# Kernel optimization log

Measured on AMD Instinct MI355X. Metric: run time of the kernel, lower is better.

The kernel has to match this reference:

```python
import jax, jax.numpy as jnp
import numpy as np

DIST = 3.0
COEFF = 10.0
NEG_SLOPE = 0.3  # keras LeakyReLU default


def _probe_points(dist=DIST):
    # fixed 26 probe offsets on a sphere of radius `dist` (from build())
    angles = np.array(
        [[j * 0.125 - 0.125, i * 0.125 + (j - 1) * 0.0625] for j in range(3) for i in range(8)]
        + [[-0.25, 0.0], [0.25, 0.0]],
        dtype=np.float32,
    ) * (2.0 * np.pi)
    a, b = angles[:, 0], angles[:, 1]
    pts = np.stack([np.sin(a), np.cos(a) * np.cos(b), np.cos(a) * np.sin(b)], axis=-1) * dist
    return jnp.asarray(pts, dtype=jnp.float32)  # (26, 3)


def setup_inputs() -> dict:
    key = jax.random.key(0)
    k1, k2, k3 = jax.random.split(key, 3)
    B, n, f = 2, 1024, 3
    m, out_feats, num_convs = 26, 6, 5
    points = jax.random.normal(k1, (B, n, 3 + f), dtype=jnp.float32)
    # per-conv Dense(m*f -> out_feats) weights/bias, stacked over num_convs
    W = jax.random.normal(k2, (num_convs, m * f, out_feats), dtype=jnp.float32) * 0.1
    b = jax.random.normal(k3, (num_convs, out_feats), dtype=jnp.float32) * 0.1
    return {"points": points, "W": W, "b": b}


def reference(points, W, b):
    B, n, df = points.shape
    d = 3
    f = df - d
    probes = _probe_points()              # (m, d)
    m = probes.shape[0]
    coords = points[..., :d]              # (B, n, d) -> centers too (l = n)
    feats = points[..., d:]               # (B, n, f)
    centers = coords
    # probes per center: (B, l, m, d)
    probes_per_center = centers[:, :, None, :] + probes[None, None, :, :]
    # delta: (B, l, m, n, d)
    delta = coords[:, None, None, :, :] - probes_per_center[:, :, :, None, :]
    sq = jnp.sum(delta * delta, axis=-1)  # (B, l, m, n)
    wgt = COEFF / (sq + COEFF)            # inverse-distance weights
    # weighted feature sum: (B, l, m, f), averaged over n
    wf = jnp.einsum('blmn,bnf->blmf', wgt, feats) / n
    x = wf.reshape(B, n, m * f)           # (B, l, m*f)
    # num_convs parallel Dense + LeakyReLU (Dropout is identity at inference)
    h = jnp.einsum('blx,kxo->blko', x, W) + b[None, None, :, :]
    h = jnp.where(h > 0, h, NEG_SLOPE * h)
    convs = h.reshape(B, n, -1)           # (B, n, num_convs*out_feats)
    return jnp.concatenate([centers, convs], axis=-1)  # (B, n, 3 + 30)
```

## Files before the change

### kernel.cpp

```cpp
#include <hip/hip_runtime.h>


#define NPROBE 26
#define NPTS   1024
#define COEFF  10.0f
#define NEG    0.3f

__device__ constexpr float PROBE[NPROBE][3] = {
  {-2.12132034f,  1.95984445f, -0.81179415f},
  {-2.12132034f,  1.95984445f,  0.81179415f},
  {-2.12132034f,  0.81179415f,  1.95984445f},
  {-2.12132034f, -0.81179415f,  1.95984445f},
  {-2.12132034f, -1.95984445f,  0.81179415f},
  {-2.12132034f, -1.95984445f, -0.81179415f},
  {-2.12132034f, -0.81179415f, -1.95984445f},
  {-2.12132034f,  0.81179415f, -1.95984445f},
  { 0.0f,         3.0f,         0.0f       },
  { 0.0f,         2.12132034f,  2.12132034f},
  { 0.0f,         0.0f,         3.0f       },
  { 0.0f,        -2.12132034f,  2.12132034f},
  { 0.0f,        -3.0f,         0.0f       },
  { 0.0f,        -2.12132034f, -2.12132034f},
  { 0.0f,         0.0f,        -3.0f       },
  { 0.0f,         2.12132034f, -2.12132034f},
  { 2.12132034f,  1.95984445f,  0.81179415f},
  { 2.12132034f,  0.81179415f,  1.95984445f},
  { 2.12132034f, -0.81179415f,  1.95984445f},
  { 2.12132034f, -1.95984445f,  0.81179415f},
  { 2.12132034f, -1.95984445f, -0.81179415f},
  { 2.12132034f, -0.81179415f, -1.95984445f},
  { 2.12132034f,  0.81179415f, -1.95984445f},
  { 2.12132034f,  1.95984445f, -0.81179415f},
  {-3.0f,         0.0f,         0.0f       },
  { 3.0f,         0.0f,         0.0f       },
};

__global__ __launch_bounds__(256) void crossconv_kernel(
    const float* __restrict__ points,
    const float* __restrict__ W,
    const float* __restrict__ bias,
    float* __restrict__ out)
{
    const int lane = threadIdx.x & 63;
    const int wid  = blockIdx.x * (blockDim.x >> 6) + (threadIdx.x >> 6);
    const int b = wid >> 10;
    const float* batch = points + b * NPTS * 6;
    const float* crow  = batch + (wid & 1023) * 6;
    const float cx = crow[0], cy = crow[1], cz = crow[2];

    float acc[NPROBE][3];
    #pragma unroll
    for (int m = 0; m < NPROBE; ++m) { acc[m][0] = 0.f; acc[m][1] = 0.f; acc[m][2] = 0.f; }

    for (int it = 0; it < NPTS / 64; ++it) {
        const float* prow = batch + (it * 64 + lane) * 6;
        const float px = prow[0], py = prow[1], pz = prow[2];
        const float f0 = prow[3], f1 = prow[4], f2 = prow[5];
        const float dx = px - cx, dy = py - cy, dz = pz - cz;
        const float base = fmaf(dx, dx, fmaf(dy, dy, fmaf(dz, dz, 19.0f)));
        #pragma unroll
        for (int m = 0; m < NPROBE; ++m) {
            float t = fmaf(-2.0f * PROBE[m][0], dx,
                      fmaf(-2.0f * PROBE[m][1], dy,
                      fmaf(-2.0f * PROBE[m][2], dz, base)));
            float w = __builtin_amdgcn_rcpf(t);
            acc[m][0] = fmaf(w, f0, acc[m][0]);
            acc[m][1] = fmaf(w, f1, acc[m][1]);
            acc[m][2] = fmaf(w, f2, acc[m][2]);
        }
    }

    #pragma unroll
    for (int m = 0; m < NPROBE; ++m) {
        #pragma unroll
        for (int ff = 0; ff < 3; ++ff) {
            float v = acc[m][ff];
            #pragma unroll
            for (int off = 32; off > 0; off >>= 1)
                v += __shfl_xor(v, off, 64);
            acc[m][ff] = v;
        }
    }

    const float scale = COEFF / (float)NPTS;
    float* orow = out + wid * 33;

    if (lane < 30) {
        const int k = lane / 6, o = lane % 6;
        const float* Wk = W + k * 78 * 6 + o;
        float h = bias[lane];
        #pragma unroll
        for (int t = 0; t < 78; ++t)
            h = fmaf(acc[t / 3][t % 3] * scale, Wk[t * 6], h);
        h = (h > 0.f) ? h : NEG * h;
        orow[3 + lane] = h;
    } else if (lane < 33) {
        orow[lane - 30] = (lane == 30) ? cx : ((lane == 31) ? cy : cz);
    }
}

extern "C" void kernel_launch(void* const* d_in, const int* in_sizes, int n_in,
                              void* d_out, int out_size, void* d_ws, size_t ws_size,
                              hipStream_t stream) {
    const float* points = (const float*)d_in[0];
    const float* W      = (const float*)d_in[1];
    const float* bias   = (const float*)d_in[2];
    float* out          = (float*)d_out;
    crossconv_kernel<<<512, 256, 0, stream>>>(points, W, bias, out);
}
```

Measured before the change: 25.79 us.

## Split probes across two waves per center and reduce with DPP

Each center is now handled by two waves, each accumulating 13 of the 26 probes, which halves the accumulator registers per thread and doubles the grid to 1024 blocks. Wave reductions switch from shuffle-xor butterflies to a DPP row/broadcast sequence that leaves the sum in lane 63. The partial sums go through shared memory so one wave can run the dense layer. Point loads are vectorised as float2, and launch bounds request 4 blocks per CU. The aims are higher occupancy and a cheaper reduction, at the cost of a block barrier and each point row being read twice per center.

```diff
diff --git a/kernel.cpp b/kernel.cpp
--- a/kernel.cpp
+++ b/kernel.cpp
@@ -1,12 +1,11 @@
 #include <hip/hip_runtime.h>
 
 
-#define NPROBE 26
 #define NPTS   1024
 #define COEFF  10.0f
 #define NEG    0.3f
 
-__device__ constexpr float PROBE[NPROBE][3] = {
+__device__ constexpr float PROBE[26][3] = {
   {-2.12132034f,  1.95984445f, -0.81179415f},
   {-2.12132034f,  1.95984445f,  0.81179415f},
   {-2.12132034f,  0.81179415f,  1.95984445f},
@@ -35,67 +34,103 @@
   { 3.0f,         0.0f,         0.0f       },
 };
 
-__global__ __launch_bounds__(256) void crossconv_kernel(
+#define DPP_STEP(x, ctrl, rm, bm, bc)                                        \
+  x += __int_as_float(__builtin_amdgcn_update_dpp(                           \
+      0, __float_as_int(x), ctrl, rm, bm, bc))
+
+__device__ __forceinline__ float wave_sum_to_lane63(float x) {
+  DPP_STEP(x, 0x111, 0xf, 0xf, true);
+  DPP_STEP(x, 0x112, 0xf, 0xf, true);
+  DPP_STEP(x, 0x114, 0xf, 0xe, false);
+  DPP_STEP(x, 0x118, 0xf, 0xc, false);
+  DPP_STEP(x, 0x142, 0xa, 0xf, false);
+  DPP_STEP(x, 0x143, 0xc, 0xf, false);
+  return x;
+}
+
+template <int OFF>
+__device__ __forceinline__ void run_main(const float* __restrict__ batch,
+                                         int lane, float cx, float cy, float cz,
+                                         float acc[13][3]) {
+  for (int it = 0; it < NPTS / 64; ++it) {
+    const float* prow = batch + (it * 64 + lane) * 6;
+    const float2 q0 = *reinterpret_cast<const float2*>(prow);
+    const float2 q1 = *reinterpret_cast<const float2*>(prow + 2);
+    const float2 q2 = *reinterpret_cast<const float2*>(prow + 4);
+    const float dx = q0.x - cx, dy = q0.y - cy, dz = q1.x - cz;
+    const float f0 = q1.y, f1 = q2.x, f2 = q2.y;
+    const float base = fmaf(dx, dx, fmaf(dy, dy, fmaf(dz, dz, 19.0f)));
+    #pragma unroll
+    for (int j = 0; j < 13; ++j) {
+      const float t = fmaf(-2.0f * PROBE[OFF + j][0], dx,
+                      fmaf(-2.0f * PROBE[OFF + j][1], dy,
+                      fmaf(-2.0f * PROBE[OFF + j][2], dz, base)));
+      const float w = __builtin_amdgcn_rcpf(t);
+      acc[j][0] = fmaf(w, f0, acc[j][0]);
+      acc[j][1] = fmaf(w, f1, acc[j][1]);
+      acc[j][2] = fmaf(w, f2, acc[j][2]);
+    }
+  }
+}
+
+__global__ __launch_bounds__(256, 4) void crossconv_kernel(
     const float* __restrict__ points,
     const float* __restrict__ W,
     const float* __restrict__ bias,
     float* __restrict__ out)
 {
-    const int lane = threadIdx.x & 63;
-    const int wid  = blockIdx.x * (blockDim.x >> 6) + (threadIdx.x >> 6);
-    const int b = wid >> 10;
-    const float* batch = points + b * NPTS * 6;
-    const float* crow  = batch + (wid & 1023) * 6;
-    const float cx = crow[0], cy = crow[1], cz = crow[2];
+    __shared__ float sx[2][78];
 
-    float acc[NPROBE][3];
+    const int tid    = threadIdx.x;
+    const int lane   = tid & 63;
+    const int w      = tid >> 6;
+    const int cLocal = w >> 1;
+    const int half   = w & 1;
+    const int G      = blockIdx.x * 2 + cLocal;
+
+    const float* batch = points + (G >> 10) * (NPTS * 6);
+    const float* crow  = points + G * 6;
+    const float  cx = crow[0], cy = crow[1], cz = crow[2];
+
+    float acc[13][3];
     #pragma unroll
-    for (int m = 0; m < NPROBE; ++m) { acc[m][0] = 0.f; acc[m][1] = 0.f; acc[m][2] = 0.f; }
+    for (int j = 0; j < 13; ++j) { acc[j][0] = 0.f; acc[j][1] = 0.f; acc[j][2] = 0.f; }
 
-    for (int it = 0; it < NPTS / 64; ++it) {
-        const float* prow = batch + (it * 64 + lane) * 6;
-        const float px = prow[0], py = prow[1], pz = prow[2];
-        const float f0 = prow[3], f1 = prow[4], f2 = prow[5];
-        const float dx = px - cx, dy = py - cy, dz = pz - cz;
-        const float base = fmaf(dx, dx, fmaf(dy, dy, fmaf(dz, dz, 19.0f)));
-        #pragma unroll
-        for (int m = 0; m < NPROBE; ++m) {
-            float t = fmaf(-2.0f * PROBE[m][0], dx,
-                      fmaf(-2.0f * PROBE[m][1], dy,
-                      fmaf(-2.0f * PROBE[m][2], dz, base)));
-            float w = __builtin_amdgcn_rcpf(t);
-            acc[m][0] = fmaf(w, f0, acc[m][0]);
-            acc[m][1] = fmaf(w, f1, acc[m][1]);
-            acc[m][2] = fmaf(w, f2, acc[m][2]);
-        }
+    if (half == 0) run_main<0>(batch, lane, cx, cy, cz, acc);
+    else           run_main<13>(batch, lane, cx, cy, cz, acc);
+
+    const float scale = COEFF / (float)NPTS;
+    #pragma unroll
+    for (int j = 0; j < 13; ++j) {
+      #pragma unroll
+      for (int ff = 0; ff < 3; ++ff)
+        acc[j][ff] = wave_sum_to_lane63(acc[j][ff]) * scale;
     }
 
-    #pragma unroll
-    for (int m = 0; m < NPROBE; ++m) {
-        #pragma unroll
-        for (int ff = 0; ff < 3; ++ff) {
-            float v = acc[m][ff];
-            #pragma unroll
-            for (int off = 32; off > 0; off >>= 1)
-                v += __shfl_xor(v, off, 64);
-            acc[m][ff] = v;
-        }
+    if (lane == 63) {
+      #pragma unroll
+      for (int j = 0; j < 13; ++j) {
+        sx[cLocal][half * 39 + j * 3 + 0] = acc[j][0];
+        sx[cLocal][half * 39 + j * 3 + 1] = acc[j][1];
+        sx[cLocal][half * 39 + j * 3 + 2] = acc[j][2];
+      }
     }
+    __syncthreads();
 
-    const float scale = COEFF / (float)NPTS;
-    float* orow = out + wid * 33;
-
-    if (lane < 30) {
+    if (half == 0) {
+      float* orow = out + G * 33;
+      if (lane < 30) {
         const int k = lane / 6, o = lane % 6;
-        const float* Wk = W + k * 78 * 6 + o;
+        const float* Wk = W + k * (78 * 6) + o;
         float h = bias[lane];
         #pragma unroll
         for (int t = 0; t < 78; ++t)
-            h = fmaf(acc[t / 3][t % 3] * scale, Wk[t * 6], h);
+          h = fmaf(sx[cLocal][t], Wk[t * 6], h);
         h = (h > 0.f) ? h : NEG * h;
         orow[3 + lane] = h;
-    } else if (lane < 33) {
+      } else if (lane < 33) {
         orow[lane - 30] = (lane == 30) ? cx : ((lane == 31) ? cy : cz);
+      }
     }
 }
 
@@ -106,5 +141,5 @@
     const float* W      = (const float*)d_in[1];
     const float* bias   = (const float*)d_in[2];
     float* out          = (float*)d_out;
-    crossconv_kernel<<<512, 256, 0, stream>>>(points, W, bias, out);
+    crossconv_kernel<<<1024, 256, 0, stream>>>(points, W, bias, out);
 }
```

Result: faster. 25.12 us (-2.6%).
